# Optimization experiments

Measured on AMD Instinct MI355X. Metric: run time of the kernel, lower is better.

The kernel has to match this reference:

```python
import jax, jax.numpy as jnp
import numpy as np

B, N, DIM_IN, DIM_OUT, EMBED, CHEB_K = 32, 2000, 64, 64, 16, 3


def setup_inputs() -> dict:
    key = jax.random.key(0)
    ks = jax.random.split(key, 6)
    return {
        "x": jax.random.normal(ks[0], (B, N, DIM_IN), dtype=jnp.float32),
        "node_embeddings": jax.random.normal(ks[1], (N, EMBED), dtype=jnp.float32),
        "nodevec1": jax.random.normal(ks[2], (N, EMBED), dtype=jnp.float32),
        "nodevec2": jax.random.normal(ks[3], (EMBED, N), dtype=jnp.float32),
        "weights_pool": jax.random.normal(ks[4], (EMBED, CHEB_K, DIM_IN, DIM_OUT), dtype=jnp.float32) * 0.1,
        "bias_pool": jax.random.normal(ks[5], (EMBED, DIM_OUT), dtype=jnp.float32) * 0.1,
    }


def reference(x, node_embeddings, nodevec1, nodevec2, weights_pool, bias_pool):
    n = node_embeddings.shape[0]
    # adaptive adjacency: softmax(relu(nodevec1 @ nodevec2)) over rows' neighbors
    s = jax.nn.softmax(jax.nn.relu(nodevec1 @ nodevec2), axis=1)  # [N, N]
    # Chebyshev polynomial stack: T0 = I, T1 = S, Tk = 2 S Tk-1 - Tk-2
    support_set = [jnp.eye(n, dtype=x.dtype), s]
    for _ in range(2, CHEB_K):
        support_set.append(2.0 * s @ support_set[-1] - support_set[-2])
    supports = jnp.stack(support_set, axis=0)  # [K, N, N]
    # node-conditioned weights / bias
    weights = jnp.einsum('nd,dkio->nkio', node_embeddings, weights_pool)  # [N, K, I, O]
    bias = node_embeddings @ bias_pool  # [N, O]
    # graph conv: aggregate then per-node combine
    x_g = jnp.einsum('knm,bmc->bnkc', supports, x)  # [B, N, K, I]
    out = jnp.einsum('bnki,nkio->bno', x_g, weights) + bias  # [B, N, O]
    return out
```

## Files before the change

### kernel.cpp

```cpp
#include <hip/hip_runtime.h>

#define N_NODES 2000
#define NP      2048
#define KB      63
#define KB3     66
#define BATCH   32
#define DIM     64
#define EMB     16
#define KI      192
#define WCOLS   12288

typedef __bf16 bf16;
typedef __attribute__((ext_vector_type(8))) __bf16 bf16x8;
typedef __attribute__((ext_vector_type(4))) float  f32x4;

struct alignas(8) bf16x4pk { bf16 v[4]; };

__device__ __forceinline__ void gl_lds16(const bf16* g, bf16* l) {
    __builtin_amdgcn_global_load_lds(
        (__attribute__((address_space(1))) void*)(g),
        (__attribute__((address_space(3))) void*)(l), 16, 0, 0);
}


#define Z0   (WCOLS * 32)
#define Z1   (Z0 + N_NODES * 32)
#define Z2   (Z1 + 3 * NP * 32)
#define PREP_SM_BLK   2554
#define PREP_BLOCKS   (N_NODES + 1024 + PREP_SM_BLK)

__global__ __launch_bounds__(256) void prep_fused(
    const float* __restrict__ nv1, const float* __restrict__ nv2,
    bf16* __restrict__ Sp,
    const float* __restrict__ X, bf16* __restrict__ Xtp, bf16* __restrict__ Xbf,
    const float* __restrict__ wp, const float* __restrict__ emb,
    bf16* __restrict__ wpT2, bf16* __restrict__ embp, bf16* __restrict__ Sp63)
{
    const int bid = blockIdx.x;
    const int tid = threadIdx.x;

    if (bid < N_NODES) {
        const int row = bid;
        const int j0  = tid * 8;
        __shared__ float sa[EMB];
        __shared__ float wred[4];
        __shared__ float bcast;
        if (tid < EMB) sa[tid] = nv1[row * EMB + tid];
        __syncthreads();

        const bool active = (tid < 250);
        float v[8] = {0,0,0,0,0,0,0,0};
        if (active) {
#pragma unroll
            for (int d = 0; d < EMB; ++d) {
                const float sd = sa[d];
                const float4 q0 = *(const float4*)&nv2[d * N_NODES + j0];
                const float4 q1 = *(const float4*)&nv2[d * N_NODES + j0 + 4];
                v[0] += sd * q0.x; v[1] += sd * q0.y; v[2] += sd * q0.z; v[3] += sd * q0.w;
                v[4] += sd * q1.x; v[5] += sd * q1.y; v[6] += sd * q1.z; v[7] += sd * q1.w;
            }
        }
        float lmax = 0.0f;
#pragma unroll
        for (int jj = 0; jj < 8; ++jj) { v[jj] = fmaxf(v[jj], 0.0f); lmax = fmaxf(lmax, v[jj]); }
#pragma unroll
        for (int off = 32; off > 0; off >>= 1)
            lmax = fmaxf(lmax, __shfl_down(lmax, off, 64));
        if ((tid & 63) == 0) wred[tid >> 6] = lmax;
        __syncthreads();
        if (tid == 0) bcast = fmaxf(fmaxf(wred[0], wred[1]), fmaxf(wred[2], wred[3]));
        __syncthreads();
        const float rmax = bcast;

        float lsum = 0.0f;
        if (active) {
#pragma unroll
            for (int jj = 0; jj < 8; ++jj) { v[jj] = __expf(v[jj] - rmax); lsum += v[jj]; }
        }
#pragma unroll
        for (int off = 32; off > 0; off >>= 1)
            lsum += __shfl_down(lsum, off, 64);
        if ((tid & 63) == 0) wred[tid >> 6] = lsum;
        __syncthreads();
        if (tid == 0) bcast = wred[0] + wred[1] + wred[2] + wred[3];
        __syncthreads();
        const float inv = 1.0f / bcast;

        if (tid < 252) {
            bf16x8 pk;
#pragma unroll
            for (int jj = 0; jj < 8; ++jj)
                pk[jj] = (bf16)(active ? v[jj] * inv : 0.0f);
            const int kb = j0 >> 5, q = (j0 >> 3) & 3;
            const int nt = row >> 6, r = row & 63;
            *(bf16x8*)&Sp[((size_t)(kb * 32 + nt) * 256 + q * 64 + r) * 8] = pk;
        }
    } else if (bid < N_NODES + 1024) {
        const int t  = bid - N_NODES;
        const int b  = t >> 5;
        const int m0 = (t & 31) * 64;
        __shared__ bf16 T[64][72];
#pragma unroll
        for (int i = 0; i < 4; ++i) {
            int idx = i * 256 + tid;
            int r  = idx >> 4;
            int c4 = (idx & 15) * 4;
            int m  = m0 + r;
            float4 v = make_float4(0.f, 0.f, 0.f, 0.f);
            if (m < N_NODES)
                v = *(const float4*)&X[((size_t)b * N_NODES + m) * DIM + c4];
            bf16x4pk pk;
            pk.v[0] = (bf16)v.x; pk.v[1] = (bf16)v.y;
            pk.v[2] = (bf16)v.z; pk.v[3] = (bf16)v.w;
            if (m < N_NODES)
                *(bf16x4pk*)&Xbf[((size_t)b * N_NODES + m) * DIM + c4] = pk;
            T[c4 + 0][r] = pk.v[0];
            T[c4 + 1][r] = pk.v[1];
            T[c4 + 2][r] = pk.v[2];
            T[c4 + 3][r] = pk.v[3];
        }
        __syncthreads();
#pragma unroll
        for (int i = 0; i < 2; ++i) {
            int idx = i * 256 + tid;
            int c   = idx >> 3;
            int mch = idx & 7;
            int kb  = (m0 >> 5) + (mch >> 2);
            if (kb < KB) {
                int q = mch & 3;
                bf16x8 vv = *(const bf16x8*)&T[c][mch * 8];
                *(bf16x8*)&Xtp[((size_t)(b * KB3 + kb) * 256 + q * 64 + c) * 8] = vv;
            }
        }
    } else {
        int idx = (bid - N_NODES - 1024) * 256 + tid;
        if (idx < Z0) {
            int col = idx >> 5, d = idx & 31;
            int o  = col / KI;
            int kk = col - o * KI;
            int cheb = kk >> 6, i = kk & 63;
            float v = (d < EMB) ? wp[(((d * 3 + cheb) * 64 + i) * 64) + o] : 0.0f;
            wpT2[idx] = (bf16)v;
        } else if (idx < Z1) {
            int j = idx - Z0;
            int n = j >> 5, d = j & 31;
            float v = (d < EMB) ? emb[n * EMB + d] : 0.0f;
            embp[j] = (bf16)v;
        } else if (idx < Z2) {
            Sp63[idx - Z1] = (bf16)0.0f;
        }
    }
}

__global__ __launch_bounds__(256, 2) void spmm_pack(
    const bf16* __restrict__ Ap, const bf16* __restrict__ Btp,
    bf16* __restrict__ Ybf, bf16* __restrict__ Ytp, int write_ytp)
{
    const int i = blockIdx.x;
    const int kx = i & 7, j = i >> 3;
    const int ntB = (j & 7) + 8 * (kx & 1);
    const int b   = ((j >> 3) << 2) + (kx >> 1);
    const int n0  = ntB * 128;
    const int tid = threadIdx.x;
    const int lane = tid & 63, wave = tid >> 6;
    const int l15 = lane & 15, quad = lane >> 4;

    __shared__ bf16 As[2][3 * 4096];
    __shared__ bf16 Bs[2][3 * 2048];

    const bf16* aslab = Ap  + (size_t)(ntB * 2) * 2048 + tid * 8;
    const bf16* bslab = Btp + (size_t)(b * KB3) * 2048 + tid * 8;

#define DMA_STAGE(buf, kb0_) {                                        \
        _Pragma("unroll")                                             \
        for (int jj = 0; jj < 3; ++jj) {                              \
            const bf16* pa = aslab + (size_t)(kb0_ + jj) * (32 * 2048);\
            const bf16* pb = bslab + (size_t)(kb0_ + jj) * 2048;      \
            gl_lds16(pa,        &As[buf][jj * 4096 + tid * 8]);       \
            gl_lds16(pa + 2048, &As[buf][jj * 4096 + 2048 + tid * 8]);\
            gl_lds16(pb,        &Bs[buf][jj * 2048 + tid * 8]);  } }

    f32x4 acc[2][4] = {};
    const int ga = (wave >> 1) * 256 + quad * 64 + (wave & 1) * 32;
    const int gb = quad * 64;

    DMA_STAGE(0, 0);
#pragma unroll 1
    for (int s = 0; s < 22; ++s) {
        const int cur = s & 1;
        __syncthreads();
        bf16x8 af[3][2], bfr[3][4];
#pragma unroll
        for (int jj = 0; jj < 3; ++jj) {
#pragma unroll
            for (int t = 0; t < 2; ++t)
                af[jj][t]  = *(const bf16x8*)&As[cur][jj * 4096 + (ga + t * 16 + l15) * 8];
#pragma unroll
            for (int t = 0; t < 4; ++t)
                bfr[jj][t] = *(const bf16x8*)&Bs[cur][jj * 2048 + (gb + t * 16 + l15) * 8];
        }
        if (s + 1 < 22) DMA_STAGE(cur ^ 1, (s + 1) * 3);
#pragma unroll
        for (int jj = 0; jj < 3; ++jj)
#pragma unroll
            for (int rt = 0; rt < 2; ++rt)
#pragma unroll
                for (int ct = 0; ct < 4; ++ct)
                    acc[rt][ct] = __builtin_amdgcn_mfma_f32_16x16x32_bf16(
                        af[jj][rt], bfr[jj][ct], acc[rt][ct], 0, 0, 0);
    }
#undef DMA_STAGE

#pragma unroll
    for (int rt = 0; rt < 2; ++rt) {
        const int nbase = n0 + wave * 32 + rt * 16 + quad * 4;
#pragma unroll
        for (int ct = 0; ct < 4; ++ct) {
            const int c = ct * 16 + l15;
#pragma unroll
            for (int r = 0; r < 4; ++r) {
                int n = nbase + r;
                if (n < N_NODES)
                    Ybf[((size_t)b * N_NODES + n) * DIM + c] = (bf16)acc[rt][ct][r];
            }
            if (write_ytp && nbase + 4 <= N_NODES) {
                const int kb2 = nbase >> 5;
                const int kq  = (nbase & 31) >> 3;
                const int j4  = nbase & 7;
                bf16x4pk pk;
                pk.v[0] = (bf16)acc[rt][ct][0];
                pk.v[1] = (bf16)acc[rt][ct][1];
                pk.v[2] = (bf16)acc[rt][ct][2];
                pk.v[3] = (bf16)acc[rt][ct][3];
                *(bf16x4pk*)&Ytp[((size_t)(b * KB3 + kb2) * 256 + kq * 64 + c) * 8 + j4] = pk;
            }
        }
    }
}

__global__ __launch_bounds__(256) void prep_W_mfma(
    const bf16* __restrict__ embp, const bf16* __restrict__ wpT2,
    bf16* __restrict__ W)
{
    const int colbase = blockIdx.x * 256;
    const int n0      = blockIdx.y * 16;
    const int tid  = threadIdx.x;
    const int lane = tid & 63, wave = tid >> 6;
    const int l15 = lane & 15, quad = lane >> 4;

    __shared__ bf16 Cs[16][264];

    const bf16x8 af = *(const bf16x8*)&embp[(n0 + l15) * 32 + quad * 8];
    const f32x4 zero = {};
#pragma unroll
    for (int ct = 0; ct < 4; ++ct) {
        const int col = colbase + wave * 64 + ct * 16 + l15;
        bf16x8 bfr = *(const bf16x8*)&wpT2[(size_t)col * 32 + quad * 8];
        f32x4 acc = __builtin_amdgcn_mfma_f32_16x16x32_bf16(af, bfr, zero, 0, 0, 0);
#pragma unroll
        for (int r = 0; r < 4; ++r)
            Cs[quad * 4 + r][wave * 64 + ct * 16 + l15] = (bf16)acc[r];
    }
    __syncthreads();
    {
        const int row = tid >> 4;
        const int c16 = (tid & 15) * 16;
        bf16x8 v0 = *(const bf16x8*)&Cs[row][c16];
        bf16x8 v1 = *(const bf16x8*)&Cs[row][c16 + 8];
        bf16* dst = &W[(size_t)(n0 + row) * WCOLS + colbase + c16];
        *(bf16x8*)dst       = v0;
        *(bf16x8*)(dst + 8) = v1;
    }
}

__global__ __launch_bounds__(256) void combine_node(
    const bf16* __restrict__ xbf, const bf16* __restrict__ y1bf,
    const bf16* __restrict__ y2bf, const float* __restrict__ emb,
    const float* __restrict__ bp, const bf16* __restrict__ W,
    float* __restrict__ out)
{
    const int n   = blockIdx.x;
    const int tid = threadIdx.x;
    const int lane = tid & 63, wave = tid >> 6;
    const int l15 = lane & 15, quad = lane >> 4;

    __shared__ bf16 As[BATCH][200];
    __shared__ bf16 Ws[DIM][200];
    __shared__ float bias_s[DIM];
    __shared__ float emb_s[EMB];

    if (tid < EMB) emb_s[tid] = emb[n * EMB + tid];

    {
        const int b  = tid >> 3;
        const int c8 = (tid & 7) * 8;
        const size_t base = ((size_t)b * N_NODES + n) * DIM + c8;
        bf16x8 vx = *(const bf16x8*)&xbf [base];
        bf16x8 v1 = *(const bf16x8*)&y1bf[base];
        bf16x8 v2 = *(const bf16x8*)&y2bf[base];
        bf16x8 p2;
#pragma unroll
        for (int e = 0; e < 8; ++e)
            p2[e] = (bf16)(2.0f * (float)v2[e] - (float)vx[e]);
        *(bf16x8*)&As[b][c8]       = vx;
        *(bf16x8*)&As[b][64 + c8]  = v1;
        *(bf16x8*)&As[b][128 + c8] = p2;
    }
    {
        const bf16* Wn = W + (size_t)n * WCOLS;
#pragma unroll
        for (int jj = 0; jj < 6; ++jj) {
            int chunk = jj * 256 + tid;
            int o  = chunk / 24;
            int kc = chunk - o * 24;
            bf16x8 v = *(const bf16x8*)&Wn[(size_t)chunk * 8];
            *(bf16x8*)&Ws[o][kc * 8] = v;
        }
    }
    __syncthreads();

    if (tid < DIM) {
        float s = 0.0f;
#pragma unroll
        for (int d = 0; d < EMB; ++d) s += emb_s[d] * bp[d * DIM + tid];
        bias_s[tid] = s;
    }

    bf16x8 af[2][6];
#pragma unroll
    for (int mt = 0; mt < 2; ++mt)
#pragma unroll
        for (int ks = 0; ks < 6; ++ks)
            af[mt][ks] = *(const bf16x8*)&As[mt * 16 + l15][ks * 32 + quad * 8];

    f32x4 acc[2] = {};
#pragma unroll
    for (int ks = 0; ks < 6; ++ks) {
        bf16x8 bfr = *(const bf16x8*)&Ws[wave * 16 + l15][ks * 32 + quad * 8];
        acc[0] = __builtin_amdgcn_mfma_f32_16x16x32_bf16(af[0][ks], bfr, acc[0], 0, 0, 0);
        acc[1] = __builtin_amdgcn_mfma_f32_16x16x32_bf16(af[1][ks], bfr, acc[1], 0, 0, 0);
    }
    __syncthreads();

    const int o = wave * 16 + l15;
    const float bv = bias_s[o];
#pragma unroll
    for (int mt = 0; mt < 2; ++mt)
#pragma unroll
        for (int r = 0; r < 4; ++r) {
            int b = mt * 16 + quad * 4 + r;
            out[((size_t)b * N_NODES + n) * DIM + o] = acc[mt][r] + bv;
        }
}

extern "C" void kernel_launch(void* const* d_in, const int* in_sizes, int n_in,
                              void* d_out, int out_size, void* d_ws, size_t ws_size,
                              hipStream_t stream) {
    const float* x   = (const float*)d_in[0];
    const float* emb = (const float*)d_in[1];
    const float* nv1 = (const float*)d_in[2];
    const float* nv2 = (const float*)d_in[3];
    const float* wp  = (const float*)d_in[4];
    const float* bp  = (const float*)d_in[5];
    float* out = (float*)d_out;

    char* w = (char*)d_ws;
    bf16* Sp   = (bf16*)w;  w += (size_t)KB3 * NP * 32 * 2;
    bf16* xTp  = (bf16*)w;  w += (size_t)BATCH * KB3 * DIM * 32 * 2;
    bf16* y1Tp = (bf16*)w;  w += (size_t)BATCH * KB3 * DIM * 32 * 2;
    bf16* xbf  = (bf16*)w;  w += (size_t)BATCH * N_NODES * DIM * 2;
    bf16* y1bf = (bf16*)w;  w += (size_t)BATCH * N_NODES * DIM * 2;
    bf16* y2bf = (bf16*)w;  w += (size_t)BATCH * N_NODES * DIM * 2;
    bf16* wpT2 = (bf16*)w;  w += (size_t)WCOLS * 32 * 2;
    bf16* embp = (bf16*)w;  w += (size_t)N_NODES * 32 * 2;
    bf16* W    = (bf16*)w;

    prep_fused<<<PREP_BLOCKS, 256, 0, stream>>>(
        nv1, nv2, Sp, x, xTp, xbf, wp, emb, wpT2, embp,
        Sp + (size_t)63 * NP * 32);
    prep_W_mfma<<<dim3(WCOLS / 256, N_NODES / 16), 256, 0, stream>>>(embp, wpT2, W);
    spmm_pack<<<512, 256, 0, stream>>>(Sp, xTp,  y1bf, y1Tp, 1);
    spmm_pack<<<512, 256, 0, stream>>>(Sp, y1Tp, y2bf, y1Tp, 0);
    combine_node<<<N_NODES, 256, 0, stream>>>(xbf, y1bf, y2bf, emb, bp, W, out);
}
```

Before: 167.4 us.

## Fuse per-node weight generation into combine kernel, dropping materialized W buffer

Removes the prep_W_mfma kernel that wrote a per-node weight tensor of 2000x12288 bf16 to global memory. The combine kernel now generates each node's weight slice on the fly, an MFMA of the node embedding against the transposed pool, staged into LDS chunk by chunk. Each block handles 8 nodes and half of the output columns, and block indices are mapped across XCDs. This avoids writing and rereading about 49MB of weights and saves one launch, at the cost of redundant weight MFMAs, wasted MFMA lanes (only 8 of 16 rows used) and more synchronization.

Measured after the change: 178.3 us. +6.5%, slower.

```diff
diff --git a/kernel.cpp b/kernel.cpp
--- a/kernel.cpp
+++ b/kernel.cpp
@@ -238,119 +238,129 @@
     }
 }
 
-__global__ __launch_bounds__(256) void prep_W_mfma(
-    const bf16* __restrict__ embp, const bf16* __restrict__ wpT2,
-    bf16* __restrict__ W)
+__global__ __launch_bounds__(256, 2) void combine_fused(
+    const bf16* __restrict__ xbf, const bf16* __restrict__ y1bf,
+    const bf16* __restrict__ y2bf, const float* __restrict__ emb,
+    const float* __restrict__ bp, const bf16* __restrict__ embp,
+    const bf16* __restrict__ wpT2, float* __restrict__ out)
 {
-    const int colbase = blockIdx.x * 256;
-    const int n0      = blockIdx.y * 16;
+    const int i   = blockIdx.x;
+    const int xcd = i & 7, j = i >> 3;
+    const int oh  = j & 1;
+    const int ng  = (j >> 1) * 8 + xcd;
+    if (ng >= 250) return;
+    const int n0  = ng * 8;
+    const int o0  = oh * 32;
+
     const int tid  = threadIdx.x;
     const int lane = tid & 63, wave = tid >> 6;
-    const int l15 = lane & 15, quad = lane >> 4;
-
-    __shared__ bf16 Cs[16][264];
-
-    const bf16x8 af = *(const bf16x8*)&embp[(n0 + l15) * 32 + quad * 8];
+    const int l15  = lane & 15, quad = lane >> 4;
+
+    __shared__ bf16  As[8 * 32 * 72];
+    __shared__ bf16  Wc[8 * 32 * 40];
+    __shared__ float bias_s[8 * 32];
+
+    {
+        const int n = tid >> 5, o = tid & 31;
+        float s = 0.0f;
+#pragma unroll
+        for (int d = 0; d < EMB; ++d)
+            s += emb[(n0 + n) * EMB + d] * bp[d * DIM + o0 + o];
+        bias_s[tid] = s;
+    }
+
+    bf16x8 af_emb;
+#pragma unroll
+    for (int e = 0; e < 8; ++e) af_emb[e] = (bf16)0.0f;
+    if (l15 < 8)
+        af_emb = *(const bf16x8*)&embp[(size_t)(n0 + l15) * 32 + quad * 8];
+
+    f32x4 acc[2][2][2] = {};
     const f32x4 zero = {};
-#pragma unroll
-    for (int ct = 0; ct < 4; ++ct) {
-        const int col = colbase + wave * 64 + ct * 16 + l15;
-        bf16x8 bfr = *(const bf16x8*)&wpT2[(size_t)col * 32 + quad * 8];
-        f32x4 acc = __builtin_amdgcn_mfma_f32_16x16x32_bf16(af, bfr, zero, 0, 0, 0);
-#pragma unroll
-        for (int r = 0; r < 4; ++r)
-            Cs[quad * 4 + r][wave * 64 + ct * 16 + l15] = (bf16)acc[r];
-    }
-    __syncthreads();
-    {
-        const int row = tid >> 4;
-        const int c16 = (tid & 15) * 16;
-        bf16x8 v0 = *(const bf16x8*)&Cs[row][c16];
-        bf16x8 v1 = *(const bf16x8*)&Cs[row][c16 + 8];
-        bf16* dst = &W[(size_t)(n0 + row) * WCOLS + colbase + c16];
-        *(bf16x8*)dst       = v0;
-        *(bf16x8*)(dst + 8) = v1;
-    }
-}
-
-__global__ __launch_bounds__(256) void combine_node(
-    const bf16* __restrict__ xbf, const bf16* __restrict__ y1bf,
-    const bf16* __restrict__ y2bf, const float* __restrict__ emb,
-    const float* __restrict__ bp, const bf16* __restrict__ W,
-    float* __restrict__ out)
-{
-    const int n   = blockIdx.x;
-    const int tid = threadIdx.x;
-    const int lane = tid & 63, wave = tid >> 6;
-    const int l15 = lane & 15, quad = lane >> 4;
-
-    __shared__ bf16 As[BATCH][200];
-    __shared__ bf16 Ws[DIM][200];
-    __shared__ float bias_s[DIM];
-    __shared__ float emb_s[EMB];
-
-    if (tid < EMB) emb_s[tid] = emb[n * EMB + tid];
-
-    {
-        const int b  = tid >> 3;
-        const int c8 = (tid & 7) * 8;
-        const size_t base = ((size_t)b * N_NODES + n) * DIM + c8;
-        bf16x8 vx = *(const bf16x8*)&xbf [base];
-        bf16x8 v1 = *(const bf16x8*)&y1bf[base];
-        bf16x8 v2 = *(const bf16x8*)&y2bf[base];
-        bf16x8 p2;
-#pragma unroll
-        for (int e = 0; e < 8; ++e)
-            p2[e] = (bf16)(2.0f * (float)v2[e] - (float)vx[e]);
-        *(bf16x8*)&As[b][c8]       = vx;
-        *(bf16x8*)&As[b][64 + c8]  = v1;
-        *(bf16x8*)&As[b][128 + c8] = p2;
-    }
-    {
-        const bf16* Wn = W + (size_t)n * WCOLS;
-#pragma unroll
-        for (int jj = 0; jj < 6; ++jj) {
-            int chunk = jj * 256 + tid;
-            int o  = chunk / 24;
-            int kc = chunk - o * 24;
-            bf16x8 v = *(const bf16x8*)&Wn[(size_t)chunk * 8];
-            *(bf16x8*)&Ws[o][kc * 8] = v;
-        }
-    }
-    __syncthreads();
-
-    if (tid < DIM) {
-        float s = 0.0f;
-#pragma unroll
-        for (int d = 0; d < EMB; ++d) s += emb_s[d] * bp[d * DIM + tid];
-        bias_s[tid] = s;
-    }
-
-    bf16x8 af[2][6];
-#pragma unroll
-    for (int mt = 0; mt < 2; ++mt)
-#pragma unroll
-        for (int ks = 0; ks < 6; ++ks)
-            af[mt][ks] = *(const bf16x8*)&As[mt * 16 + l15][ks * 32 + quad * 8];
-
-    f32x4 acc[2] = {};
-#pragma unroll
-    for (int ks = 0; ks < 6; ++ks) {
-        bf16x8 bfr = *(const bf16x8*)&Ws[wave * 16 + l15][ks * 32 + quad * 8];
-        acc[0] = __builtin_amdgcn_mfma_f32_16x16x32_bf16(af[0][ks], bfr, acc[0], 0, 0, 0);
-        acc[1] = __builtin_amdgcn_mfma_f32_16x16x32_bf16(af[1][ks], bfr, acc[1], 0, 0, 0);
-    }
-    __syncthreads();
-
-    const int o = wave * 16 + l15;
-    const float bv = bias_s[o];
-#pragma unroll
-    for (int mt = 0; mt < 2; ++mt)
-#pragma unroll
-        for (int r = 0; r < 4; ++r) {
-            int b = mt * 16 + quad * 4 + r;
-            out[((size_t)b * N_NODES + n) * DIM + o] = acc[mt][r] + bv;
-        }
+
+    const int sb  = tid >> 3;
+    const int sln = tid & 7;
+
+    for (int s = 0; s < 3; ++s) {
+        {
+            const size_t slab = ((size_t)sb * N_NODES + n0) * DIM;
+            if (s == 0 || s == 1) {
+                const bf16* src = (s == 0) ? xbf : y1bf;
+#pragma unroll
+                for (int jj = 0; jj < 8; ++jj) {
+                    const int f = jj * 8 + sln;
+                    const int n = f >> 3, c8 = f & 7;
+                    bf16x8 v = *(const bf16x8*)&src[slab + f * 8];
+                    *(bf16x8*)&As[(n * 32 + sb) * 72 + c8 * 8] = v;
+                }
+            } else {
+#pragma unroll
+                for (int jj = 0; jj < 8; ++jj) {
+                    const int f = jj * 8 + sln;
+                    const int n = f >> 3, c8 = f & 7;
+                    bf16x8 v2 = *(const bf16x8*)&y2bf[slab + f * 8];
+                    bf16x8 vx = *(const bf16x8*)&xbf [slab + f * 8];
+                    bf16x8 p;
+#pragma unroll
+                    for (int e = 0; e < 8; ++e)
+                        p[e] = (bf16)(2.0f * (float)v2[e] - (float)vx[e]);
+                    *(bf16x8*)&As[(n * 32 + sb) * 72 + c8 * 8] = p;
+                }
+            }
+        }
+        __syncthreads();
+
+#pragma unroll
+        for (int ch = 0; ch < 2; ++ch) {
+#pragma unroll
+            for (int u = 0; u < 16; ++u) {
+                const int o  = wave * 8 + (u >> 1);
+                const int kt = u & 1;
+                const int col = (o0 + o) * KI + s * 64 + ch * 32 + kt * 16 + l15;
+                bf16x8 bfr = *(const bf16x8*)&wpT2[(size_t)col * 32 + quad * 8];
+                f32x4 c = __builtin_amdgcn_mfma_f32_16x16x32_bf16(
+                    af_emb, bfr, zero, 0, 0, 0);
+                if (quad < 2) {
+#pragma unroll
+                    for (int r = 0; r < 4; ++r)
+                        Wc[((quad * 4 + r) * 32 + o) * 40 + kt * 16 + l15] = (bf16)c[r];
+                }
+            }
+            __syncthreads();
+
+#pragma unroll
+            for (int np = 0; np < 2; ++np) {
+                const int n = wave * 2 + np;
+                bf16x8 a0 = *(const bf16x8*)&As[(n * 32 +      l15) * 72 + ch * 32 + quad * 8];
+                bf16x8 a1 = *(const bf16x8*)&As[(n * 32 + 16 + l15) * 72 + ch * 32 + quad * 8];
+                bf16x8 b0 = *(const bf16x8*)&Wc[(n * 32 +      l15) * 40 + quad * 8];
+                bf16x8 b1 = *(const bf16x8*)&Wc[(n * 32 + 16 + l15) * 40 + quad * 8];
+                acc[np][0][0] = __builtin_amdgcn_mfma_f32_16x16x32_bf16(a0, b0, acc[np][0][0], 0, 0, 0);
+                acc[np][0][1] = __builtin_amdgcn_mfma_f32_16x16x32_bf16(a0, b1, acc[np][0][1], 0, 0, 0);
+                acc[np][1][0] = __builtin_amdgcn_mfma_f32_16x16x32_bf16(a1, b0, acc[np][1][0], 0, 0, 0);
+                acc[np][1][1] = __builtin_amdgcn_mfma_f32_16x16x32_bf16(a1, b1, acc[np][1][1], 0, 0, 0);
+            }
+            __syncthreads();
+        }
+    }
+
+#pragma unroll
+    for (int np = 0; np < 2; ++np) {
+        const int nl = wave * 2 + np;
+        const int n  = n0 + nl;
+#pragma unroll
+        for (int mt = 0; mt < 2; ++mt)
+#pragma unroll
+            for (int nt = 0; nt < 2; ++nt) {
+                const int o  = o0 + nt * 16 + l15;
+                const float bv = bias_s[nl * 32 + nt * 16 + l15];
+#pragma unroll
+                for (int r = 0; r < 4; ++r) {
+                    const int b = mt * 16 + quad * 4 + r;
+                    out[((size_t)b * N_NODES + n) * DIM + o] = acc[np][mt][nt][r] + bv;
+                }
+            }
+    }
 }
 
 extern "C" void kernel_launch(void* const* d_in, const int* in_sizes, int n_in,
@@ -372,14 +382,12 @@
     bf16* y1bf = (bf16*)w;  w += (size_t)BATCH * N_NODES * DIM * 2;
     bf16* y2bf = (bf16*)w;  w += (size_t)BATCH * N_NODES * DIM * 2;
     bf16* wpT2 = (bf16*)w;  w += (size_t)WCOLS * 32 * 2;
-    bf16* embp = (bf16*)w;  w += (size_t)N_NODES * 32 * 2;
-    bf16* W    = (bf16*)w;
+    bf16* embp = (bf16*)w;
 
     prep_fused<<<PREP_BLOCKS, 256, 0, stream>>>(
         nv1, nv2, Sp, x, xTp, xbf, wp, emb, wpT2, embp,
         Sp + (size_t)63 * NP * 32);
-    prep_W_mfma<<<dim3(WCOLS / 256, N_NODES / 16), 256, 0, stream>>>(embp, wpT2, W);
     spmm_pack<<<512, 256, 0, stream>>>(Sp, xTp,  y1bf, y1Tp, 1);
     spmm_pack<<<512, 256, 0, stream>>>(Sp, y1Tp, y2bf, y1Tp, 0);
-    combine_node<<<N_NODES, 256, 0, stream>>>(xbf, y1bf, y2bf, emb, bp, W, out);
-}
+    combine_fused<<<512, 256, 0, stream>>>(xbf, y1bf, y2bf, emb, bp, embp, wpT2, out);
+}
```

## Fuse W-generation blocks into first SpMM launch to overlap independent work

Applied to the files above, without the earlier changes.

Merges the prep_W_mfma grid into the first SpMM kernel as extra blocks, so the W generation runs alongside the first Chebyshev aggregation in a single launch. The first SpMM is rewritten with two-step double buffering (48KB LDS) and targets 3 blocks per CU, down from 3-step stages. This removes one launch and fills idle CUs during the 512-block SpMM tail, at the cost of a larger, divergent kernel whose LDS footprint may limit occupancy for the tiny W blocks.

Measured after the change: 162.1 us. 1.03x faster.

```diff
diff --git a/kernel.cpp b/kernel.cpp
--- a/kernel.cpp
+++ b/kernel.cpp
@@ -152,9 +152,129 @@
     }
 }
 
+__global__ __launch_bounds__(256, 3) void spmm1_plus(
+    const bf16* __restrict__ Ap, const bf16* __restrict__ Btp,
+    bf16* __restrict__ Ybf, bf16* __restrict__ Ytp,
+    const bf16* __restrict__ embp, const bf16* __restrict__ wpT2,
+    bf16* __restrict__ W)
+{
+    __shared__ __align__(16) char smem[49152];
+    const int bid  = blockIdx.x;
+    const int tid  = threadIdx.x;
+    const int lane = tid & 63, wave = tid >> 6;
+    const int l15  = lane & 15, quad = lane >> 4;
+
+    if (bid < 512) {
+        bf16* As = (bf16*)smem;
+        bf16* Bs = (bf16*)(smem + 32768);
+
+        const int kx = bid & 7, j = bid >> 3;
+        const int ntB = (j & 7) + 8 * (kx & 1);
+        const int b   = ((j >> 3) << 2) + (kx >> 1);
+        const int n0  = ntB * 128;
+
+        const bf16* aslab = Ap  + (size_t)(ntB * 2) * 2048 + tid * 8;
+        const bf16* bslab = Btp + (size_t)(b * KB3) * 2048 + tid * 8;
+
+#define DMA_STAGE2(buf, kb0_) {                                          \
+        _Pragma("unroll")                                                \
+        for (int jj = 0; jj < 2; ++jj) {                                 \
+            const bf16* pa = aslab + (size_t)(kb0_ + jj) * (32 * 2048);  \
+            const bf16* pb = bslab + (size_t)(kb0_ + jj) * 2048;         \
+            gl_lds16(pa,        &As[(buf) * 8192 + jj * 4096 + tid * 8]);        \
+            gl_lds16(pa + 2048, &As[(buf) * 8192 + jj * 4096 + 2048 + tid * 8]); \
+            gl_lds16(pb,        &Bs[(buf) * 4096 + jj * 2048 + tid * 8]);  } }
+
+        f32x4 acc[2][4] = {};
+        const int ga = (wave >> 1) * 256 + quad * 64 + (wave & 1) * 32;
+        const int gb = quad * 64;
+
+        DMA_STAGE2(0, 0);
+#pragma unroll 1
+        for (int s = 0; s < 33; ++s) {
+            const int cur = s & 1;
+            __syncthreads();
+            bf16x8 af[2][2], bfr[2][4];
+#pragma unroll
+            for (int jj = 0; jj < 2; ++jj) {
+#pragma unroll
+                for (int t = 0; t < 2; ++t)
+                    af[jj][t]  = *(const bf16x8*)&As[cur * 8192 + jj * 4096 + (ga + t * 16 + l15) * 8];
+#pragma unroll
+                for (int t = 0; t < 4; ++t)
+                    bfr[jj][t] = *(const bf16x8*)&Bs[cur * 4096 + jj * 2048 + (gb + t * 16 + l15) * 8];
+            }
+            if (s + 1 < 33) DMA_STAGE2(cur ^ 1, (s + 1) * 2);
+#pragma unroll
+            for (int jj = 0; jj < 2; ++jj)
+#pragma unroll
+                for (int rt = 0; rt < 2; ++rt)
+#pragma unroll
+                    for (int ct = 0; ct < 4; ++ct)
+                        acc[rt][ct] = __builtin_amdgcn_mfma_f32_16x16x32_bf16(
+                            af[jj][rt], bfr[jj][ct], acc[rt][ct], 0, 0, 0);
+        }
+#undef DMA_STAGE2
+
+#pragma unroll
+        for (int rt = 0; rt < 2; ++rt) {
+            const int nbase = n0 + wave * 32 + rt * 16 + quad * 4;
+#pragma unroll
+            for (int ct = 0; ct < 4; ++ct) {
+                const int c = ct * 16 + l15;
+#pragma unroll
+                for (int r = 0; r < 4; ++r) {
+                    int n = nbase + r;
+                    if (n < N_NODES)
+                        Ybf[((size_t)b * N_NODES + n) * DIM + c] = (bf16)acc[rt][ct][r];
+                }
+                if (nbase + 4 <= N_NODES) {
+                    const int kb2 = nbase >> 5;
+                    const int kq  = (nbase & 31) >> 3;
+                    const int j4  = nbase & 7;
+                    bf16x4pk pk;
+                    pk.v[0] = (bf16)acc[rt][ct][0];
+                    pk.v[1] = (bf16)acc[rt][ct][1];
+                    pk.v[2] = (bf16)acc[rt][ct][2];
+                    pk.v[3] = (bf16)acc[rt][ct][3];
+                    *(bf16x4pk*)&Ytp[((size_t)(b * KB3 + kb2) * 256 + kq * 64 + c) * 8 + j4] = pk;
+                }
+            }
+        }
+    } else {
+        bf16 (*Cs)[264] = (bf16(*)[264])smem;
+
+        const int pid     = bid - 512;
+        const int colbase = (pid % 48) * 256;
+        const int n0      = (pid / 48) * 16;
+
+        const bf16x8 af = *(const bf16x8*)&embp[(n0 + l15) * 32 + quad * 8];
+        const f32x4 zero = {};
+#pragma unroll
+        for (int ct = 0; ct < 4; ++ct) {
+            const int col = colbase + wave * 64 + ct * 16 + l15;
+            bf16x8 bfr = *(const bf16x8*)&wpT2[(size_t)col * 32 + quad * 8];
+            f32x4 acc = __builtin_amdgcn_mfma_f32_16x16x32_bf16(af, bfr, zero, 0, 0, 0);
+#pragma unroll
+            for (int r = 0; r < 4; ++r)
+                Cs[quad * 4 + r][wave * 64 + ct * 16 + l15] = (bf16)acc[r];
+        }
+        __syncthreads();
+        {
+            const int row = tid >> 4;
+            const int c16 = (tid & 15) * 16;
+            bf16x8 v0 = *(const bf16x8*)&Cs[row][c16];
+            bf16x8 v1 = *(const bf16x8*)&Cs[row][c16 + 8];
+            bf16* dst = &W[(size_t)(n0 + row) * WCOLS + colbase + c16];
+            *(bf16x8*)dst       = v0;
+            *(bf16x8*)(dst + 8) = v1;
+        }
+    }
+}
+
 __global__ __launch_bounds__(256, 2) void spmm_pack(
     const bf16* __restrict__ Ap, const bf16* __restrict__ Btp,
-    bf16* __restrict__ Ybf, bf16* __restrict__ Ytp, int write_ytp)
+    bf16* __restrict__ Ybf)
 {
     const int i = blockIdx.x;
     const int kx = i & 7, j = i >> 3;
@@ -223,53 +343,7 @@
                 if (n < N_NODES)
                     Ybf[((size_t)b * N_NODES + n) * DIM + c] = (bf16)acc[rt][ct][r];
             }
-            if (write_ytp && nbase + 4 <= N_NODES) {
-                const int kb2 = nbase >> 5;
-                const int kq  = (nbase & 31) >> 3;
-                const int j4  = nbase & 7;
-                bf16x4pk pk;
-                pk.v[0] = (bf16)acc[rt][ct][0];
-                pk.v[1] = (bf16)acc[rt][ct][1];
-                pk.v[2] = (bf16)acc[rt][ct][2];
-                pk.v[3] = (bf16)acc[rt][ct][3];
-                *(bf16x4pk*)&Ytp[((size_t)(b * KB3 + kb2) * 256 + kq * 64 + c) * 8 + j4] = pk;
-            }
-        }
-    }
-}
-
-__global__ __launch_bounds__(256) void prep_W_mfma(
-    const bf16* __restrict__ embp, const bf16* __restrict__ wpT2,
-    bf16* __restrict__ W)
-{
-    const int colbase = blockIdx.x * 256;
-    const int n0      = blockIdx.y * 16;
-    const int tid  = threadIdx.x;
-    const int lane = tid & 63, wave = tid >> 6;
-    const int l15 = lane & 15, quad = lane >> 4;
-
-    __shared__ bf16 Cs[16][264];
-
-    const bf16x8 af = *(const bf16x8*)&embp[(n0 + l15) * 32 + quad * 8];
-    const f32x4 zero = {};
-#pragma unroll
-    for (int ct = 0; ct < 4; ++ct) {
-        const int col = colbase + wave * 64 + ct * 16 + l15;
-        bf16x8 bfr = *(const bf16x8*)&wpT2[(size_t)col * 32 + quad * 8];
-        f32x4 acc = __builtin_amdgcn_mfma_f32_16x16x32_bf16(af, bfr, zero, 0, 0, 0);
-#pragma unroll
-        for (int r = 0; r < 4; ++r)
-            Cs[quad * 4 + r][wave * 64 + ct * 16 + l15] = (bf16)acc[r];
-    }
-    __syncthreads();
-    {
-        const int row = tid >> 4;
-        const int c16 = (tid & 15) * 16;
-        bf16x8 v0 = *(const bf16x8*)&Cs[row][c16];
-        bf16x8 v1 = *(const bf16x8*)&Cs[row][c16 + 8];
-        bf16* dst = &W[(size_t)(n0 + row) * WCOLS + colbase + c16];
-        *(bf16x8*)dst       = v0;
-        *(bf16x8*)(dst + 8) = v1;
+        }
     }
 }
 
@@ -378,8 +452,7 @@
     prep_fused<<<PREP_BLOCKS, 256, 0, stream>>>(
         nv1, nv2, Sp, x, xTp, xbf, wp, emb, wpT2, embp,
         Sp + (size_t)63 * NP * 32);
-    prep_W_mfma<<<dim3(WCOLS / 256, N_NODES / 16), 256, 0, stream>>>(embp, wpT2, W);
-    spmm_pack<<<512, 256, 0, stream>>>(Sp, xTp,  y1bf, y1Tp, 1);
-    spmm_pack<<<512, 256, 0, stream>>>(Sp, y1Tp, y2bf, y1Tp, 0);
+    spmm1_plus<<<512 + 6000, 256, 0, stream>>>(Sp, xTp, y1bf, y1Tp, embp, wpT2, W);
+    spmm_pack<<<512, 256, 0, stream>>>(Sp, y1Tp, y2bf);
     combine_node<<<N_NODES, 256, 0, stream>>>(xbf, y1bf, y2bf, emb, bp, W, out);
 }
```

## Fuse per-node weight generation into prep kernel and triple-buffer SpMM pipeline

Applied to the files above, without the earlier changes.

Removes the separate prep_W_mfma launch and the intermediate transposed weight/embedding buffers. Prep blocks now read the fp32 weights_pool and embeddings directly, convert them in registers, and compute 5 node groups per block. The SpMM kernel moves from a 2-stage double buffer of 3 k-blocks to a 3-stage ring of 2 k-blocks, using explicit vmcnt waits so two DMA stages stay in flight. The aim is lower launch overhead and better latency hiding, at the cost of strided fp32 gathers in prep and more fragile hand-written waitcnt logic.

Result: slower. 190.2 us (+13.7%).

```diff
diff --git a/kernel.cpp b/kernel.cpp
--- a/kernel.cpp
+++ b/kernel.cpp
@@ -23,18 +23,16 @@
 }
 
 
-#define Z0   (WCOLS * 32)
-#define Z1   (Z0 + N_NODES * 32)
-#define Z2   (Z1 + 3 * NP * 32)
-#define PREP_SM_BLK   2554
-#define PREP_BLOCKS   (N_NODES + 1024 + PREP_SM_BLK)
+#define ZERO_BLK  96
+#define PW_BLOCKS 1200
+#define PREP_BLOCKS (N_NODES + 1024 + ZERO_BLK + PW_BLOCKS)
 
 __global__ __launch_bounds__(256) void prep_fused(
     const float* __restrict__ nv1, const float* __restrict__ nv2,
     bf16* __restrict__ Sp,
     const float* __restrict__ X, bf16* __restrict__ Xtp, bf16* __restrict__ Xbf,
     const float* __restrict__ wp, const float* __restrict__ emb,
-    bf16* __restrict__ wpT2, bf16* __restrict__ embp, bf16* __restrict__ Sp63)
+    bf16* __restrict__ W, bf16* __restrict__ Sp63)
 {
     const int bid = blockIdx.x;
     const int tid = threadIdx.x;
@@ -132,27 +130,79 @@
                 *(bf16x8*)&Xtp[((size_t)(b * KB3 + kb) * 256 + q * 64 + c) * 8] = vv;
             }
         }
+    } else if (bid < N_NODES + 1024 + ZERO_BLK) {
+        const int idx = (bid - N_NODES - 1024) * 256 + tid;
+        bf16x8 z;
+#pragma unroll
+        for (int e = 0; e < 8; ++e) z[e] = (bf16)0.0f;
+        *(bf16x8*)&Sp63[(size_t)idx * 8] = z;
     } else {
-        int idx = (bid - N_NODES - 1024) * 256 + tid;
-        if (idx < Z0) {
-            int col = idx >> 5, d = idx & 31;
-            int o  = col / KI;
-            int kk = col - o * KI;
-            int cheb = kk >> 6, i = kk & 63;
-            float v = (d < EMB) ? wp[(((d * 3 + cheb) * 64 + i) * 64) + o] : 0.0f;
-            wpT2[idx] = (bf16)v;
-        } else if (idx < Z1) {
-            int j = idx - Z0;
-            int n = j >> 5, d = j & 31;
-            float v = (d < EMB) ? emb[n * EMB + d] : 0.0f;
-            embp[j] = (bf16)v;
-        } else if (idx < Z2) {
-            Sp63[idx - Z1] = (bf16)0.0f;
+        __shared__ bf16 CsW[16][264];
+        const int pid     = bid - (N_NODES + 1024 + ZERO_BLK);
+        const int colbase = (pid % 48) * 256;
+        const int ng0     = (pid / 48) * 5;
+
+        const int lane = tid & 63, wave = tid >> 6;
+        const int l15 = lane & 15, quad = lane >> 4;
+
+        bf16x8 bfr[4];
+#pragma unroll
+        for (int ct = 0; ct < 4; ++ct) {
+            const int col  = colbase + wave * 64 + ct * 16 + l15;
+            const int o    = col / KI;
+            const int kk   = col - o * KI;
+            const int cheb = kk >> 6, ii = kk & 63;
+            bf16x8 v;
+#pragma unroll
+            for (int e = 0; e < 8; ++e) v[e] = (bf16)0.0f;
+            if (quad < 2) {
+                const float* base = &wp[((((quad * 8) * 3 + cheb) * 64 + ii) * 64) + o];
+#pragma unroll
+                for (int e = 0; e < 8; ++e)
+                    v[e] = (bf16)base[(size_t)e * (3 * 64 * 64)];
+            }
+            bfr[ct] = v;
+        }
+        bf16x8 afs[5];
+#pragma unroll
+        for (int g = 0; g < 5; ++g) {
+            bf16x8 v;
+#pragma unroll
+            for (int e = 0; e < 8; ++e) v[e] = (bf16)0.0f;
+            if (quad < 2) {
+                const float* base = &emb[((ng0 + g) * 16 + l15) * EMB + quad * 8];
+#pragma unroll
+                for (int e = 0; e < 8; ++e) v[e] = (bf16)base[e];
+            }
+            afs[g] = v;
+        }
+        const f32x4 zero = {};
+#pragma unroll
+        for (int g = 0; g < 5; ++g) {
+            const int n0 = (ng0 + g) * 16;
+#pragma unroll
+            for (int ct = 0; ct < 4; ++ct) {
+                f32x4 acc = __builtin_amdgcn_mfma_f32_16x16x32_bf16(afs[g], bfr[ct], zero, 0, 0, 0);
+#pragma unroll
+                for (int r = 0; r < 4; ++r)
+                    CsW[quad * 4 + r][wave * 64 + ct * 16 + l15] = (bf16)acc[r];
+            }
+            __syncthreads();
+            {
+                const int row = tid >> 4;
+                const int c16 = (tid & 15) * 16;
+                bf16x8 v0 = *(const bf16x8*)&CsW[row][c16];
+                bf16x8 v1 = *(const bf16x8*)&CsW[row][c16 + 8];
+                bf16* dst = &W[(size_t)(n0 + row) * WCOLS + colbase + c16];
+                *(bf16x8*)dst       = v0;
+                *(bf16x8*)(dst + 8) = v1;
+            }
+            __syncthreads();
         }
     }
 }
 
-__global__ __launch_bounds__(256, 2) void spmm_pack(
+__global__ __launch_bounds__(256, 2) void spmm_pipe(
     const bf16* __restrict__ Ap, const bf16* __restrict__ Btp,
     bf16* __restrict__ Ybf, bf16* __restrict__ Ytp, int write_ytp)
 {
@@ -165,33 +215,44 @@
     const int lane = tid & 63, wave = tid >> 6;
     const int l15 = lane & 15, quad = lane >> 4;
 
-    __shared__ bf16 As[2][3 * 4096];
-    __shared__ bf16 Bs[2][3 * 2048];
+    __shared__ bf16 As[3][2 * 4096];
+    __shared__ bf16 Bs[3][2 * 2048];
 
     const bf16* aslab = Ap  + (size_t)(ntB * 2) * 2048 + tid * 8;
     const bf16* bslab = Btp + (size_t)(b * KB3) * 2048 + tid * 8;
 
-#define DMA_STAGE(buf, kb0_) {                                        \
-        _Pragma("unroll")                                             \
-        for (int jj = 0; jj < 3; ++jj) {                              \
-            const bf16* pa = aslab + (size_t)(kb0_ + jj) * (32 * 2048);\
-            const bf16* pb = bslab + (size_t)(kb0_ + jj) * 2048;      \
-            gl_lds16(pa,        &As[buf][jj * 4096 + tid * 8]);       \
-            gl_lds16(pa + 2048, &As[buf][jj * 4096 + 2048 + tid * 8]);\
-            gl_lds16(pb,        &Bs[buf][jj * 2048 + tid * 8]);  } }
+#define STAGE(buf, s_) {                                               \
+        _Pragma("unroll")                                              \
+        for (int jj = 0; jj < 2; ++jj) {                               \
+            const bf16* pa = aslab + (size_t)(2 * (s_) + jj) * (32 * 2048); \
+            const bf16* pb = bslab + (size_t)(2 * (s_) + jj) * 2048;   \
+            gl_lds16(pa,        &As[buf][jj * 4096 + tid * 8]);        \
+            gl_lds16(pa + 2048, &As[buf][jj * 4096 + 2048 + tid * 8]); \
+            gl_lds16(pb,        &Bs[buf][jj * 2048 + tid * 8]); } }
 
     f32x4 acc[2][4] = {};
     const int ga = (wave >> 1) * 256 + quad * 64 + (wave & 1) * 32;
     const int gb = quad * 64;
 
-    DMA_STAGE(0, 0);
+    STAGE(0, 0);
+    STAGE(1, 1);
 #pragma unroll 1
-    for (int s = 0; s < 22; ++s) {
-        const int cur = s & 1;
-        __syncthreads();
-        bf16x8 af[3][2], bfr[3][4];
-#pragma unroll
-        for (int jj = 0; jj < 3; ++jj) {
+    for (int s = 0; s < 33; ++s) {
+        const int cur = s % 3;
+        if (s + 1 < 33) {
+            asm volatile("s_waitcnt vmcnt(6)" ::: "memory");
+        } else {
+            asm volatile("s_waitcnt vmcnt(0)" ::: "memory");
+        }
+        __builtin_amdgcn_s_barrier();
+        __builtin_amdgcn_sched_barrier(0);
+        if (s + 2 < 33) {
+            const int nxt = (cur + 2 >= 3) ? cur - 1 : cur + 2;
+            STAGE(nxt, s + 2);
+        }
+        bf16x8 af[2][2], bfr[2][4];
+#pragma unroll
+        for (int jj = 0; jj < 2; ++jj) {
 #pragma unroll
             for (int t = 0; t < 2; ++t)
                 af[jj][t]  = *(const bf16x8*)&As[cur][jj * 4096 + (ga + t * 16 + l15) * 8];
@@ -199,9 +260,8 @@
             for (int t = 0; t < 4; ++t)
                 bfr[jj][t] = *(const bf16x8*)&Bs[cur][jj * 2048 + (gb + t * 16 + l15) * 8];
         }
-        if (s + 1 < 22) DMA_STAGE(cur ^ 1, (s + 1) * 3);
-#pragma unroll
-        for (int jj = 0; jj < 3; ++jj)
+#pragma unroll
+        for (int jj = 0; jj < 2; ++jj)
 #pragma unroll
             for (int rt = 0; rt < 2; ++rt)
 #pragma unroll
@@ -209,7 +269,7 @@
                     acc[rt][ct] = __builtin_amdgcn_mfma_f32_16x16x32_bf16(
                         af[jj][rt], bfr[jj][ct], acc[rt][ct], 0, 0, 0);
     }
-#undef DMA_STAGE
+#undef STAGE
 
 #pragma unroll
     for (int rt = 0; rt < 2; ++rt) {
@@ -238,41 +298,6 @@
     }
 }
 
-__global__ __launch_bounds__(256) void prep_W_mfma(
-    const bf16* __restrict__ embp, const bf16* __restrict__ wpT2,
-    bf16* __restrict__ W)
-{
-    const int colbase = blockIdx.x * 256;
-    const int n0      = blockIdx.y * 16;
-    const int tid  = threadIdx.x;
-    const int lane = tid & 63, wave = tid >> 6;
-    const int l15 = lane & 15, quad = lane >> 4;
-
-    __shared__ bf16 Cs[16][264];
-
-    const bf16x8 af = *(const bf16x8*)&embp[(n0 + l15) * 32 + quad * 8];
-    const f32x4 zero = {};
-#pragma unroll
-    for (int ct = 0; ct < 4; ++ct) {
-        const int col = colbase + wave * 64 + ct * 16 + l15;
-        bf16x8 bfr = *(const bf16x8*)&wpT2[(size_t)col * 32 + quad * 8];
-        f32x4 acc = __builtin_amdgcn_mfma_f32_16x16x32_bf16(af, bfr, zero, 0, 0, 0);
-#pragma unroll
-        for (int r = 0; r < 4; ++r)
-            Cs[quad * 4 + r][wave * 64 + ct * 16 + l15] = (bf16)acc[r];
-    }
-    __syncthreads();
-    {
-        const int row = tid >> 4;
-        const int c16 = (tid & 15) * 16;
-        bf16x8 v0 = *(const bf16x8*)&Cs[row][c16];
-        bf16x8 v1 = *(const bf16x8*)&Cs[row][c16 + 8];
-        bf16* dst = &W[(size_t)(n0 + row) * WCOLS + colbase + c16];
-        *(bf16x8*)dst       = v0;
-        *(bf16x8*)(dst + 8) = v1;
-    }
-}
-
 __global__ __launch_bounds__(256) void combine_node(
     const bf16* __restrict__ xbf, const bf16* __restrict__ y1bf,
     const bf16* __restrict__ y2bf, const float* __restrict__ emb,
@@ -371,15 +396,12 @@
     bf16* xbf  = (bf16*)w;  w += (size_t)BATCH * N_NODES * DIM * 2;
     bf16* y1bf = (bf16*)w;  w += (size_t)BATCH * N_NODES * DIM * 2;
     bf16* y2bf = (bf16*)w;  w += (size_t)BATCH * N_NODES * DIM * 2;
-    bf16* wpT2 = (bf16*)w;  w += (size_t)WCOLS * 32 * 2;
-    bf16* embp = (bf16*)w;  w += (size_t)N_NODES * 32 * 2;
     bf16* W    = (bf16*)w;
 
     prep_fused<<<PREP_BLOCKS, 256, 0, stream>>>(
-        nv1, nv2, Sp, x, xTp, xbf, wp, emb, wpT2, embp,
+        nv1, nv2, Sp, x, xTp, xbf, wp, emb, W,
         Sp + (size_t)63 * NP * 32);
-    prep_W_mfma<<<dim3(WCOLS / 256, N_NODES / 16), 256, 0, stream>>>(embp, wpT2, W);
-    spmm_pack<<<512, 256, 0, stream>>>(Sp, xTp,  y1bf, y1Tp, 1);
-    spmm_pack<<<512, 256, 0, stream>>>(Sp, y1Tp, y2bf, y1Tp, 0);
+    spmm_pipe<<<512, 256, 0, stream>>>(Sp, xTp,  y1bf, y1Tp, 1);
+    spmm_pipe<<<512, 256, 0, stream>>>(Sp, y1Tp, y2bf, y1Tp, 0);
     combine_node<<<N_NODES, 256, 0, stream>>>(xbf, y1bf, y2bf, emb, bp, W, out);
 }
```
